# Kernel tuning notes

Measured on AMD Instinct MI355X. Metric: run time of the kernel, lower is better.

Reference implementation:

```python
import jax, jax.numpy as jnp
import numpy as np

S, D, H, DK, DV = 2048, 1024, 16, 64, 64


def setup_inputs() -> dict:
    key = jax.random.key(0)
    ks = jax.random.split(key, 7)
    sc = 1.0 / np.sqrt(D)
    return {
        "encodings_for_q": jax.random.normal(ks[0], (S, D), jnp.float32),
        "encodings_for_k": jax.random.normal(ks[1], (S, D), jnp.float32),
        "encodings_for_v": jax.random.normal(ks[2], (S, D), jnp.float32),
        # per-head projection weights, stacked over heads (math-equivalent to
        # num_heads separate bias-free nn.Linear layers)
        "W_q": jax.random.normal(ks[3], (H, D, DK), jnp.float32) * sc,
        "W_k": jax.random.normal(ks[4], (H, D, DK), jnp.float32) * sc,
        "W_v": jax.random.normal(ks[5], (H, D, DV), jnp.float32) * sc,
        "W_out": jax.random.normal(ks[6], (H * DV, D), jnp.float32) * sc,
    }


def reference(encodings_for_q, encodings_for_k, encodings_for_v, W_q, W_k, W_v, W_out):
    # per-head projections: [H, S, dk/dv]
    q = jnp.einsum("sd,hdk->hsk", encodings_for_q, W_q)
    k = jnp.einsum("sd,hdk->hsk", encodings_for_k, W_k)
    v = jnp.einsum("sd,hdv->hsv", encodings_for_v, W_v)
    # scaled dot-product attention; scale = sqrt(d_k) (k.size(col_dim))
    sims = jnp.einsum("hsk,htk->hst", q, k) / jnp.sqrt(jnp.asarray(DK, q.dtype))
    attn = jax.nn.softmax(sims, axis=-1)
    ctx = jnp.einsum("hst,htv->hsv", attn, v)  # [H, S, dv]
    # concat heads along feature dim (head-major order, like torch.cat)
    cat = jnp.transpose(ctx, (1, 0, 2)).reshape(S, H * DV)
    return cat @ W_out
```

## Files before the change

### kernel.cpp

```cpp
#include <hip/hip_runtime.h>
#include <hip/hip_bf16.h>

typedef __attribute__((ext_vector_type(8))) short bf16x8;
typedef __attribute__((ext_vector_type(4))) float f32x4;

#define S_  2048
#define D_  1024
#define H_  16
#define QK_SCALE 0.18033688011f

__device__ __forceinline__ unsigned short f2bf(float x) {
    union { float f; unsigned u; } v; v.f = x;
    unsigned r = v.u + 0x7fffu + ((v.u >> 16) & 1u);
    return (unsigned short)(r >> 16);
}

__device__ __forceinline__ float bf2f(unsigned short s) {
    union { unsigned u; float f; } v; v.u = (unsigned)s << 16; return v.f;
}

__device__ __forceinline__ unsigned short bfbits(float x) {
    union { __hip_bfloat16 h; unsigned short s; } c;
    c.h = __float2bfloat16(x);
    return c.s;
}

__device__ __forceinline__ float fexp2(float x) {
#if __has_builtin(__builtin_amdgcn_exp2f)
    return __builtin_amdgcn_exp2f(x);
#else
    float r;
    asm("v_exp_f32 %0, %1" : "=v"(r) : "v"(x));
    return r;
#endif
}

__device__ __forceinline__ void gload16(const unsigned short* g, unsigned short* l) {
    __builtin_amdgcn_global_load_lds((const __attribute__((address_space(1))) void*)g,
                                     (__attribute__((address_space(3))) void*)l, 16, 0, 0);
}

__device__ __forceinline__ void drain_vm() {
    asm volatile("s_waitcnt vmcnt(0)" ::: "memory");
}

__global__ __launch_bounds__(256) void prep(
    const float* __restrict__ eq, const float* __restrict__ ek, const float* __restrict__ ev,
    const float* __restrict__ wq, const float* __restrict__ wk, const float* __restrict__ wv,
    const float* __restrict__ wo,
    unsigned short* __restrict__ oeq, unsigned short* __restrict__ oek,
    unsigned short* __restrict__ oev, unsigned short* __restrict__ owq,
    unsigned short* __restrict__ owk, unsigned short* __restrict__ owv,
    unsigned short* __restrict__ owo) {
    const int bx = blockIdx.x, tid = threadIdx.x;
    if (bx < 6144) {
        const float* in = bx < 2048 ? eq : bx < 4096 ? ek : ev;
        unsigned short* out = bx < 2048 ? oeq : bx < 4096 ? oek : oev;
        int i = (bx & 2047) * 256 + tid;
        float4 v = ((const float4*)in)[i];
        ushort4 o;
        o.x = f2bf(v.x); o.y = f2bf(v.y); o.z = f2bf(v.z); o.w = f2bf(v.w);
        ((ushort4*)out)[i] = o;
        return;
    }
    __shared__ float t[32][33];
    const int tx = tid & 31, ty = tid >> 5;
    if (bx < 9216) {
        int idx = bx - 6144;
        int zh = idx >> 6, rem = idx & 63;
        int which = zh >> 4, h = zh & 15;
        const float* I = (which == 0 ? wq : which == 1 ? wk : wv) + (long)h * 65536;
        unsigned short* O = (which == 0 ? owq : which == 1 ? owk : owv) + (long)h * 65536;
        float sc = which == 0 ? QK_SCALE : 1.0f;
        int c0 = (rem >> 5) * 32, r0 = (rem & 31) * 32;
        #pragma unroll
        for (int r = 0; r < 4; ++r)
            t[ty + r * 8][tx] = I[(long)(r0 + ty + r * 8) * 64 + c0 + tx];
        __syncthreads();
        #pragma unroll
        for (int r = 0; r < 4; ++r)
            O[(long)(c0 + ty + r * 8) * 1024 + r0 + tx] = f2bf(sc * t[tx][ty + r * 8]);
    } else {
        int idx = bx - 9216;
        int c0 = (idx >> 5) * 32, r0 = (idx & 31) * 32;
        #pragma unroll
        for (int r = 0; r < 4; ++r)
            t[ty + r * 8][tx] = wo[(long)(r0 + ty + r * 8) * 1024 + c0 + tx];
        __syncthreads();
        #pragma unroll
        for (int r = 0; r < 4; ++r)
            owo[(long)(c0 + ty + r * 8) * 1024 + r0 + tx] = f2bf(t[tx][ty + r * 8]);
    }
}

template<int MODE>
__device__ __forceinline__ void gemm64x128(unsigned short (*As)[64 * 64],
                                           unsigned short (*Bs)[128 * 64],
                                           const unsigned short* __restrict__ A,
                                           const unsigned short* __restrict__ Bt,
                                           void* __restrict__ C, int m0, int n0, int ldc) {
    const int tid = threadIdx.x, wv = tid >> 6, lane = tid & 63, lg = lane >> 4, lr = lane & 15;
    f32x4 acc[4][2] = {};
    const unsigned short* Ab = A + (size_t)m0 * D_;
    const unsigned short* Bb = Bt + (size_t)n0 * D_;
    auto stage = [&](int b, int kt) {
        #pragma unroll
        for (int it = 0; it < 2; ++it) {
            int c = it * 256 + wv * 64 + lane;
            int row = c >> 3, jj = (c & 7) ^ (row & 7);
            gload16(Ab + (size_t)row * D_ + kt * 64 + jj * 8, &As[b][(it * 256 + wv * 64) * 8]);
        }
        #pragma unroll
        for (int it = 0; it < 4; ++it) {
            int c = it * 256 + wv * 64 + lane;
            int row = c >> 3, jj = (c & 7) ^ (row & 7);
            gload16(Bb + (size_t)row * D_ + kt * 64 + jj * 8, &Bs[b][(it * 256 + wv * 64) * 8]);
        }
    };
    stage(0, 0);
    drain_vm();
    __syncthreads();
    int buf = 0;
    for (int kt = 0; kt < 16; ++kt) {
        if (kt + 1 < 16) stage(buf ^ 1, kt + 1);
        #pragma unroll
        for (int kk = 0; kk < 2; ++kk) {
            bf16x8 af[4], bfr[2];
            #pragma unroll
            for (int mf = 0; mf < 4; ++mf) {
                int r = mf * 16 + lr;
                af[mf] = *(const bf16x8*)&As[buf][(r * 8 + ((kk * 4 + lg) ^ (r & 7))) * 8];
            }
            #pragma unroll
            for (int nf = 0; nf < 2; ++nf) {
                int r = wv * 32 + nf * 16 + lr;
                bfr[nf] = *(const bf16x8*)&Bs[buf][(r * 8 + ((kk * 4 + lg) ^ (r & 7))) * 8];
            }
            #pragma unroll
            for (int mf = 0; mf < 4; ++mf)
                #pragma unroll
                for (int nf = 0; nf < 2; ++nf)
                    acc[mf][nf] = __builtin_amdgcn_mfma_f32_16x16x32_bf16(af[mf], bfr[nf], acc[mf][nf], 0, 0, 0);
        }
        drain_vm();
        __syncthreads();
        buf ^= 1;
    }
    #pragma unroll
    for (int mf = 0; mf < 4; ++mf)
        #pragma unroll
        for (int nf = 0; nf < 2; ++nf) {
            if (MODE == 1) {
                int gn = n0 + wv * 32 + nf * 16 + lr;
                int pg = m0 + (mf >> 1) * 32 + lg * 8 + (mf & 1) * 4;
                ushort4 pk;
                pk.x = f2bf(acc[mf][nf][0]); pk.y = f2bf(acc[mf][nf][1]);
                pk.z = f2bf(acc[mf][nf][2]); pk.w = f2bf(acc[mf][nf][3]);
                *(ushort4*)&((unsigned short*)C)[(size_t)gn * ldc + pg] = pk;
            } else {
                #pragma unroll
                for (int j = 0; j < 4; ++j) {
                    int gm = m0 + mf * 16 + lg * 4 + j;
                    int gn = n0 + wv * 32 + nf * 16 + lr;
                    ((unsigned short*)C)[(size_t)gm * ldc + gn] = f2bf(acc[mf][nf][j]);
                }
            }
        }
}

__global__ __launch_bounds__(256, 3) void proj_kernel(
    const unsigned short* __restrict__ Eq, const unsigned short* __restrict__ Ek,
    const unsigned short* __restrict__ Ev, const unsigned short* __restrict__ Wqt,
    const unsigned short* __restrict__ Wkt, const unsigned short* __restrict__ Wvt,
    unsigned short* __restrict__ Qb, unsigned short* __restrict__ Kb,
    unsigned short* __restrict__ Vtb) {
    __shared__ alignas(16) unsigned short As[2][64 * 64];
    __shared__ alignas(16) unsigned short Bs[2][128 * 64];
    int m0 = blockIdx.x * 64, n0 = blockIdx.y * 128;
    if (blockIdx.z == 0)      gemm64x128<0>(As, Bs, Eq, Wqt, Qb, m0, n0, 1024);
    else if (blockIdx.z == 1) gemm64x128<0>(As, Bs, Ek, Wkt, Kb, m0, n0, 1024);
    else                      gemm64x128<1>(As, Bs, Ev, Wvt, Vtb, m0, n0, S_);
}

__global__ __launch_bounds__(256, 2) void out_gemm(const unsigned short* __restrict__ Cat,
                                                   const unsigned short* __restrict__ Wot,
                                                   float* __restrict__ Out) {
    __shared__ alignas(16) unsigned short As[2][64 * 64];
    __shared__ alignas(16) unsigned short Bs[2][64 * 64];
    const int tid = threadIdx.x, wv = tid >> 6, lane = tid & 63, lg = lane >> 4, lr = lane & 15;
    int m0 = blockIdx.x * 64, n0 = blockIdx.y * 64;
    f32x4 acc[4] = {};
    const unsigned short* Ab = Cat + (size_t)m0 * D_;
    const unsigned short* Bb = Wot + (size_t)n0 * D_;
    auto stage = [&](int b, int kt) {
        #pragma unroll
        for (int it = 0; it < 2; ++it) {
            int c = it * 256 + wv * 64 + lane;
            int row = c >> 3, jj = (c & 7) ^ (row & 7);
            gload16(Ab + (size_t)row * D_ + kt * 64 + jj * 8, &As[b][(it * 256 + wv * 64) * 8]);
        }
        #pragma unroll
        for (int it = 0; it < 2; ++it) {
            int c = it * 256 + wv * 64 + lane;
            int row = c >> 3, jj = (c & 7) ^ (row & 7);
            gload16(Bb + (size_t)row * D_ + kt * 64 + jj * 8, &Bs[b][(it * 256 + wv * 64) * 8]);
        }
    };
    stage(0, 0);
    drain_vm();
    __syncthreads();
    int buf = 0;
    for (int kt = 0; kt < 16; ++kt) {
        if (kt + 1 < 16) stage(buf ^ 1, kt + 1);
        #pragma unroll
        for (int kk = 0; kk < 2; ++kk) {
            int ra = wv * 16 + lr;
            bf16x8 af = *(const bf16x8*)&As[buf][(ra * 8 + ((kk * 4 + lg) ^ (ra & 7))) * 8];
            #pragma unroll
            for (int nf = 0; nf < 4; ++nf) {
                int r = nf * 16 + lr;
                bf16x8 bfr = *(const bf16x8*)&Bs[buf][(r * 8 + ((kk * 4 + lg) ^ (r & 7))) * 8];
                acc[nf] = __builtin_amdgcn_mfma_f32_16x16x32_bf16(af, bfr, acc[nf], 0, 0, 0);
            }
        }
        drain_vm();
        __syncthreads();
        buf ^= 1;
    }
    #pragma unroll
    for (int nf = 0; nf < 4; ++nf)
        #pragma unroll
        for (int j = 0; j < 4; ++j)
            Out[(size_t)(m0 + wv * 16 + lg * 4 + j) * 1024 + n0 + nf * 16 + lr] = acc[nf][j];
}

__global__ __launch_bounds__(128, 2) void attn_kernel(
    const unsigned short* __restrict__ Qb, const unsigned short* __restrict__ Kb,
    const unsigned short* __restrict__ Vtb, unsigned short* __restrict__ Opb,
    float* __restrict__ Lsum) {
    __shared__ alignas(16) unsigned short Ks[2][64 * 64];
    __shared__ alignas(16) unsigned short Vs[2][64 * 64];

    const int h = blockIdx.y, s0 = blockIdx.x * 128, z = blockIdx.z;
    const int tid = threadIdx.x, wv = tid >> 6, lane = tid & 63, lg = lane >> 4, lr = lane & 15;

    bf16x8 q0[4], q1[4];
    #pragma unroll
    for (int st = 0; st < 4; ++st) {
        const unsigned short* qr = Qb + (size_t)(s0 + wv * 64 + st * 16 + lr) * D_ + h * 64;
        q0[st] = *(const bf16x8*)(qr + lg * 8);
        q1[st] = *(const bf16x8*)(qr + 32 + lg * 8);
    }

    float l[4] = {0.f, 0.f, 0.f, 0.f};
    f32x4 o[4][4] = {};

    const unsigned short* KhB = Kb + h * 64;
    const unsigned short* VhB = Vtb + (size_t)(h * 64) * S_;
    const int t0 = z * 8;

    auto stageL = [&](int u) {
        int t = t0 + u, slot = u & 1;
        #pragma unroll
        for (int it = 0; it < 4; ++it) {
            int c = it * 128 + tid;
            int row = c >> 3, jj = (c & 7) ^ (row & 7);
            gload16(KhB + (size_t)(t * 64 + row) * D_ + jj * 8, &Ks[slot][c * 8]);
        }
        #pragma unroll
        for (int it = 0; it < 4; ++it) {
            int c = it * 128 + tid;
            int row = c >> 3, jj = (c & 7) ^ (row & 7);
            gload16(VhB + (size_t)row * S_ + t * 64 + jj * 8, &Vs[slot][c * 8]);
        }
    };

    stageL(0);
    #pragma unroll
    for (int tt = 0; tt < 8; ++tt) {
        if (tt + 1 < 8) {
            stageL(tt + 1);
            asm volatile("s_waitcnt vmcnt(8)" ::: "memory");
        } else {
            asm volatile("s_waitcnt vmcnt(0)" ::: "memory");
        }
        __builtin_amdgcn_s_barrier();

        const unsigned short* K_ = Ks[tt & 1];
        const unsigned short* V_ = Vs[tt & 1];

        f32x4 s[4][4];
        __builtin_amdgcn_s_setprio(1);
        #pragma unroll
        for (int kk = 0; kk < 2; ++kk)
            #pragma unroll
            for (int n = 0; n < 4; ++n) {
                int r = n * 16 + lr;
                bf16x8 kf = *(const bf16x8*)&K_[(r * 8 + ((kk * 4 + lg) ^ (r & 7))) * 8];
                #pragma unroll
                for (int st = 0; st < 4; ++st) {
                    if (kk == 0) {
                        f32x4 zz = {};
                        s[st][n] = __builtin_amdgcn_mfma_f32_16x16x32_bf16(kf, q0[st], zz, 0, 0, 0);
                    } else {
                        s[st][n] = __builtin_amdgcn_mfma_f32_16x16x32_bf16(kf, q1[st], s[st][n], 0, 0, 0);
                    }
                }
            }
        __builtin_amdgcn_s_setprio(0);

        bf16x8 p[4][2];
        #pragma unroll
        for (int st = 0; st < 4; ++st) {
            float rs = 0.f;
            #pragma unroll
            for (int n = 0; n < 4; ++n)
                #pragma unroll
                for (int j = 0; j < 4; ++j) {
                    float pv = fexp2(s[st][n][j]);
                    s[st][n][j] = pv; rs += pv;
                }
            l[st] += rs;
            #pragma unroll
            for (int kk = 0; kk < 2; ++kk) {
                union { bf16x8 v; unsigned short u[8]; } t_;
                #pragma unroll
                for (int i = 0; i < 4; ++i) {
                    t_.u[i]     = bfbits(s[st][2 * kk][i]);
                    t_.u[4 + i] = bfbits(s[st][2 * kk + 1][i]);
                }
                p[st][kk] = t_.v;
            }
        }
        __builtin_amdgcn_s_setprio(1);
        #pragma unroll
        for (int n = 0; n < 4; ++n) {
            int r = n * 16 + lr;
            #pragma unroll
            for (int kk = 0; kk < 2; ++kk) {
                bf16x8 vf = *(const bf16x8*)&V_[(r * 8 + ((kk * 4 + lg) ^ (r & 7))) * 8];
                #pragma unroll
                for (int st = 0; st < 4; ++st)
                    o[st][n] = __builtin_amdgcn_mfma_f32_16x16x32_bf16(vf, p[st][kk], o[st][n], 0, 0, 0);
            }
        }
        __builtin_amdgcn_s_setprio(0);
        __builtin_amdgcn_s_barrier();
    }
    #pragma unroll
    for (int st = 0; st < 4; ++st) {
        l[st] += __shfl_xor(l[st], 16);
        l[st] += __shfl_xor(l[st], 32);
    }
    const int slot = z * 16 + h;
    #pragma unroll
    for (int st = 0; st < 4; ++st) {
        size_t q = (size_t)s0 + wv * 64 + st * 16 + lr;
        size_t base = ((size_t)slot * S_ + q) * 64;
        #pragma unroll
        for (int n = 0; n < 4; ++n) {
            ushort4 pk;
            pk.x = f2bf(o[st][n][0]); pk.y = f2bf(o[st][n][1]);
            pk.z = f2bf(o[st][n][2]); pk.w = f2bf(o[st][n][3]);
            *(ushort4*)&Opb[base + n * 16 + lg * 4] = pk;
        }
        if (lg == 0)
            Lsum[(size_t)slot * S_ + q] = l[st];
    }
}

__global__ __launch_bounds__(256) void combine(const unsigned short* __restrict__ Opb,
                                               const float* __restrict__ Lsum,
                                               unsigned short* __restrict__ Cat) {
    int gid = blockIdx.x * 256 + threadIdx.x;
    int d4 = gid & 15, s = (gid >> 4) & 2047, h = gid >> 15;
    float denom = 0.f;
    #pragma unroll
    for (int i = 0; i < 4; ++i)
        denom += Lsum[(size_t)(i * 16 + h) * S_ + s];
    float inv = 1.f / fmaxf(denom, 1e-30f);
    float o0 = 0.f, o1 = 0.f, o2 = 0.f, o3 = 0.f;
    #pragma unroll
    for (int i = 0; i < 4; ++i) {
        ushort4 u = *(const ushort4*)&Opb[((size_t)(i * 16 + h) * S_ + s) * 64 + d4 * 4];
        o0 += bf2f(u.x); o1 += bf2f(u.y);
        o2 += bf2f(u.z); o3 += bf2f(u.w);
    }
    ushort4 pk;
    pk.x = f2bf(o0 * inv); pk.y = f2bf(o1 * inv);
    pk.z = f2bf(o2 * inv); pk.w = f2bf(o3 * inv);
    *(ushort4*)&Cat[(size_t)s * D_ + h * 64 + d4 * 4] = pk;
}

extern "C" void kernel_launch(void* const* d_in, const int* in_sizes, int n_in,
                              void* d_out, int out_size, void* d_ws, size_t ws_size,
                              hipStream_t stream) {
    const float* enc_q = (const float*)d_in[0];
    const float* enc_k = (const float*)d_in[1];
    const float* enc_v = (const float*)d_in[2];
    const float* W_q   = (const float*)d_in[3];
    const float* W_k   = (const float*)d_in[4];
    const float* W_v   = (const float*)d_in[5];
    const float* W_out = (const float*)d_in[6];
    float* out = (float*)d_out;

    const size_t M1 = 1024 * 1024;
    unsigned short* Eqb = (unsigned short*)d_ws;
    unsigned short* Ekb = Eqb + 2 * M1;
    unsigned short* Evb = Ekb + 2 * M1;
    unsigned short* Wqt = Evb + 2 * M1;
    unsigned short* Wkt = Wqt + M1;
    unsigned short* Wvt = Wkt + M1;
    unsigned short* Wot = Wvt + M1;
    unsigned short* Qb  = Wot + M1;
    unsigned short* Kb  = Qb  + 2 * M1;
    unsigned short* Vtb = Kb  + 2 * M1;
    unsigned short* Cat = Vtb + 2 * M1;
    unsigned short* Opb = (unsigned short*)d_ws;
    float* Lsum = (float*)((char*)d_ws + 17u * 1024 * 1024);

    prep<<<10240, 256, 0, stream>>>(enc_q, enc_k, enc_v, W_q, W_k, W_v, W_out,
                                    Eqb, Ekb, Evb, Wqt, Wkt, Wvt, Wot);
    proj_kernel<<<dim3(32, 8, 3), 256, 0, stream>>>(Eqb, Ekb, Evb, Wqt, Wkt, Wvt, Qb, Kb, Vtb);
    attn_kernel<<<dim3(16, 16, 4), 128, 0, stream>>>(Qb, Kb, Vtb, Opb, Lsum);
    combine<<<2048, 256, 0, stream>>>(Opb, Lsum, Cat);
    out_gemm<<<dim3(32, 16), 256, 0, stream>>>(Cat, Wot, out);
}
```

Measured before the change: 84.17 us.

## Fuse split-K attention combine into output GEMM and triple-buffer attention K/V

Removes the separate combine kernel and the Cat buffer. The output GEMM now loads the four partial attention outputs and their row sums, normalizes them in registers and writes the bf16 A tile to shared memory itself. The attention kernel also moves from double to triple buffering of K/V tiles, prefetching two tiles ahead. This saves a launch and a round trip of Cat through global memory. In exchange the out_gemm A loads are redundant across its 16 column blocks (four times the bytes per tile), and the extra LDS in the attention kernel may reduce occupancy.

Measured after the change: 232.1 us. 176% more time.

```diff
diff --git a/kernel.cpp b/kernel.cpp
--- a/kernel.cpp
+++ b/kernel.cpp
@@ -182,23 +182,55 @@
     else                      gemm64x128<1>(As, Bs, Ev, Wvt, Vtb, m0, n0, S_);
 }
 
-__global__ __launch_bounds__(256, 2) void out_gemm(const unsigned short* __restrict__ Cat,
+__global__ __launch_bounds__(256, 2) void out_gemm(const unsigned short* __restrict__ Opb,
+                                                   const float* __restrict__ Lsum,
                                                    const unsigned short* __restrict__ Wot,
                                                    float* __restrict__ Out) {
     __shared__ alignas(16) unsigned short As[2][64 * 64];
     __shared__ alignas(16) unsigned short Bs[2][64 * 64];
+    __shared__ float dInv[16][64];
     const int tid = threadIdx.x, wv = tid >> 6, lane = tid & 63, lg = lane >> 4, lr = lane & 15;
     int m0 = blockIdx.x * 64, n0 = blockIdx.y * 64;
-    f32x4 acc[4] = {};
-    const unsigned short* Ab = Cat + (size_t)m0 * D_;
     const unsigned short* Bb = Wot + (size_t)n0 * D_;
-    auto stage = [&](int b, int kt) {
-        #pragma unroll
-        for (int it = 0; it < 2; ++it) {
-            int c = it * 256 + wv * 64 + lane;
-            int row = c >> 3, jj = (c & 7) ^ (row & 7);
-            gload16(Ab + (size_t)row * D_ + kt * 64 + jj * 8, &As[b][(it * 256 + wv * 64) * 8]);
-        }
+
+    #pragma unroll
+    for (int v = 0; v < 4; ++v) {
+        int idx = tid * 4 + v;
+        int kt = idx >> 6, row = idx & 63;
+        float d = 0.f;
+        #pragma unroll
+        for (int i = 0; i < 4; ++i)
+            d += Lsum[(size_t)((i * 16 + kt) * S_) + m0 + row];
+        dInv[kt][row] = 1.f / fmaxf(d, 1e-30f);
+    }
+
+    const int c0 = 2 * tid;
+    const int arow = c0 >> 3, aj = c0 & 7;
+
+    auto aload = [&](int kt, uint4* L) {
+        #pragma unroll
+        for (int ch = 0; ch < 2; ++ch)
+            #pragma unroll
+            for (int i = 0; i < 4; ++i)
+                L[ch * 4 + i] = *(const uint4*)&Opb[((size_t)((i * 16 + kt) * S_) + m0 + arow) * 64 + (aj + ch) * 8];
+    };
+    auto acombine = [&](int kt, const uint4* L, int b) {
+        float inv = dInv[kt][arow];
+        #pragma unroll
+        for (int ch = 0; ch < 2; ++ch) {
+            union { bf16x8 v; unsigned short u[8]; ushort4 h4[2]; } src[4], dst;
+            #pragma unroll
+            for (int i = 0; i < 4; ++i) *(uint4*)&src[i] = L[ch * 4 + i];
+            #pragma unroll
+            for (int e = 0; e < 8; ++e) {
+                float s = bf2f(src[0].u[e]) + bf2f(src[1].u[e]) + bf2f(src[2].u[e]) + bf2f(src[3].u[e]);
+                dst.u[e] = f2bf(s * inv);
+            }
+            int slot = arow * 8 + ((aj + ch) ^ (arow & 7));
+            *(bf16x8*)&As[b][slot * 8] = dst.v;
+        }
+    };
+    auto stageB = [&](int b, int kt) {
         #pragma unroll
         for (int it = 0; it < 2; ++it) {
             int c = it * 256 + wv * 64 + lane;
@@ -206,12 +238,21 @@
             gload16(Bb + (size_t)row * D_ + kt * 64 + jj * 8, &Bs[b][(it * 256 + wv * 64) * 8]);
         }
     };
-    stage(0, 0);
-    drain_vm();
+
+    f32x4 acc[4] = {};
+    uint4 la[8], lb[8];
+    aload(0, la);
+    stageB(0, 0);
+    __syncthreads();
+    acombine(0, la, 0);
     __syncthreads();
     int buf = 0;
     for (int kt = 0; kt < 16; ++kt) {
-        if (kt + 1 < 16) stage(buf ^ 1, kt + 1);
+        uint4* lnext = (kt & 1) ? la : lb;
+        if (kt + 1 < 16) {
+            aload(kt + 1, lnext);
+            stageB(buf ^ 1, kt + 1);
+        }
         #pragma unroll
         for (int kk = 0; kk < 2; ++kk) {
             int ra = wv * 16 + lr;
@@ -223,7 +264,7 @@
                 acc[nf] = __builtin_amdgcn_mfma_f32_16x16x32_bf16(af, bfr, acc[nf], 0, 0, 0);
             }
         }
-        drain_vm();
+        if (kt + 1 < 16) acombine(kt + 1, lnext, buf ^ 1);
         __syncthreads();
         buf ^= 1;
     }
@@ -238,8 +279,8 @@
     const unsigned short* __restrict__ Qb, const unsigned short* __restrict__ Kb,
     const unsigned short* __restrict__ Vtb, unsigned short* __restrict__ Opb,
     float* __restrict__ Lsum) {
-    __shared__ alignas(16) unsigned short Ks[2][64 * 64];
-    __shared__ alignas(16) unsigned short Vs[2][64 * 64];
+    __shared__ alignas(16) unsigned short Ks[3][64 * 64];
+    __shared__ alignas(16) unsigned short Vs[3][64 * 64];
 
     const int h = blockIdx.y, s0 = blockIdx.x * 128, z = blockIdx.z;
     const int tid = threadIdx.x, wv = tid >> 6, lane = tid & 63, lg = lane >> 4, lr = lane & 15;
@@ -260,7 +301,7 @@
     const int t0 = z * 8;
 
     auto stageL = [&](int u) {
-        int t = t0 + u, slot = u & 1;
+        int t = t0 + u, slot = u % 3;
         #pragma unroll
         for (int it = 0; it < 4; ++it) {
             int c = it * 128 + tid;
@@ -276,18 +317,21 @@
     };
 
     stageL(0);
+    stageL(1);
     #pragma unroll
     for (int tt = 0; tt < 8; ++tt) {
-        if (tt + 1 < 8) {
-            stageL(tt + 1);
+        if (tt + 2 < 8) {
+            stageL(tt + 2);
+            asm volatile("s_waitcnt vmcnt(16)" ::: "memory");
+        } else if (tt + 1 < 8) {
             asm volatile("s_waitcnt vmcnt(8)" ::: "memory");
         } else {
             asm volatile("s_waitcnt vmcnt(0)" ::: "memory");
         }
         __builtin_amdgcn_s_barrier();
 
-        const unsigned short* K_ = Ks[tt & 1];
-        const unsigned short* V_ = Vs[tt & 1];
+        const unsigned short* K_ = Ks[tt % 3];
+        const unsigned short* V_ = Vs[tt % 3];
 
         f32x4 s[4][4];
         __builtin_amdgcn_s_setprio(1);
@@ -367,29 +411,6 @@
         if (lg == 0)
             Lsum[(size_t)slot * S_ + q] = l[st];
     }
-}
-
-__global__ __launch_bounds__(256) void combine(const unsigned short* __restrict__ Opb,
-                                               const float* __restrict__ Lsum,
-                                               unsigned short* __restrict__ Cat) {
-    int gid = blockIdx.x * 256 + threadIdx.x;
-    int d4 = gid & 15, s = (gid >> 4) & 2047, h = gid >> 15;
-    float denom = 0.f;
-    #pragma unroll
-    for (int i = 0; i < 4; ++i)
-        denom += Lsum[(size_t)(i * 16 + h) * S_ + s];
-    float inv = 1.f / fmaxf(denom, 1e-30f);
-    float o0 = 0.f, o1 = 0.f, o2 = 0.f, o3 = 0.f;
-    #pragma unroll
-    for (int i = 0; i < 4; ++i) {
-        ushort4 u = *(const ushort4*)&Opb[((size_t)(i * 16 + h) * S_ + s) * 64 + d4 * 4];
-        o0 += bf2f(u.x); o1 += bf2f(u.y);
-        o2 += bf2f(u.z); o3 += bf2f(u.w);
-    }
-    ushort4 pk;
-    pk.x = f2bf(o0 * inv); pk.y = f2bf(o1 * inv);
-    pk.z = f2bf(o2 * inv); pk.w = f2bf(o3 * inv);
-    *(ushort4*)&Cat[(size_t)s * D_ + h * 64 + d4 * 4] = pk;
 }
 
 extern "C" void kernel_launch(void* const* d_in, const int* in_sizes, int n_in,
@@ -415,7 +436,6 @@
     unsigned short* Qb  = Wot + M1;
     unsigned short* Kb  = Qb  + 2 * M1;
     unsigned short* Vtb = Kb  + 2 * M1;
-    unsigned short* Cat = Vtb + 2 * M1;
     unsigned short* Opb = (unsigned short*)d_ws;
     float* Lsum = (float*)((char*)d_ws + 17u * 1024 * 1024);
 
@@ -423,6 +443,5 @@
                                     Eqb, Ekb, Evb, Wqt, Wkt, Wvt, Wot);
     proj_kernel<<<dim3(32, 8, 3), 256, 0, stream>>>(Eqb, Ekb, Evb, Wqt, Wkt, Wvt, Qb, Kb, Vtb);
     attn_kernel<<<dim3(16, 16, 4), 128, 0, stream>>>(Qb, Kb, Vtb, Opb, Lsum);
-    combine<<<2048, 256, 0, stream>>>(Opb, Lsum, Cat);
-    out_gemm<<<dim3(32, 16), 256, 0, stream>>>(Cat, Wot, out);
-}
+    out_gemm<<<dim3(32, 16), 256, 0, stream>>>(Opb, Lsum, Wot, out);
+}
```
